# Kernel optimization log

Hardware: AMD Instinct MI355X
Metric: run time of the kernel (lower is better)

Reference implementation:

```python
import jax, jax.numpy as jnp
import numpy as np

B, H, T, D = 2, 16, 2048, 64


def setup_inputs() -> dict:
    key = jax.random.key(0)
    kq, kk, kv, km = jax.random.split(key, 4)
    q = jax.random.normal(kq, (B, H, T, D), dtype=jnp.float32)
    k = jax.random.normal(kk, (B, H, T, D), dtype=jnp.float32)
    v = jax.random.normal(kv, (B, H, T, D), dtype=jnp.float32)
    # boolean mask, True = masked out (broadcast over batch and heads)
    mask = jax.random.randint(km, (1, 1, T, T), 0, 2).astype(jnp.bool_)
    return {"q": q, "k": k, "v": v, "mask": mask}


def reference(q, k, v, mask):
    scale = q.shape[-1] ** (-0.5)
    # [B,H,T,T] score matrix (materialized, as in the original)
    scores = jnp.einsum("bhqd,bhkd->bhqk", q, k) * scale
    scores = jnp.where(mask, jnp.float32(-10000.0), scores)
    attn = jax.nn.softmax(scores, axis=-1)
    attn = jnp.where(mask, jnp.float32(0.0), attn)
    return jnp.einsum("bhqk,bhkd->bhqd", attn, v)
```

## Files before the change

kernel.cpp:

```cpp
#include <hip/hip_runtime.h>
#include <hip/hip_bf16.h>

typedef __bf16 bf16x8 __attribute__((ext_vector_type(8)));
typedef __bf16 bf16x4 __attribute__((ext_vector_type(4)));
typedef float  f32x4  __attribute__((ext_vector_type(4)));

#define T_SEQ 2048
#define D_HEAD 64
#define BH_N 32
#define NT_TILES (T_SEQ / 64)
#define QT_N 32
#define IMG_BYTES 16384
#define SCALE_LOG2 0.18033688011112042f

#define WS_IMG ((size_t)0)
#define WS_MB  ((size_t)16u << 20)

static __device__ __forceinline__ f32x4 mfma32(bf16x8 a, bf16x8 b, f32x4 c) {
    return __builtin_amdgcn_mfma_f32_16x16x32_bf16(a, b, c, 0, 0, 0);
}

static __device__ __forceinline__ float fast_exp2(float x) {
#if __has_builtin(__builtin_amdgcn_exp2f)
    return __builtin_amdgcn_exp2f(x);
#else
    return exp2f(x);
#endif
}

static __device__ __forceinline__ void gload16(const void* g, void* l, int lane) {
#if __has_builtin(__builtin_amdgcn_global_load_lds)
    (void)lane;
    __builtin_amdgcn_global_load_lds(
        (const __attribute__((address_space(1))) void*)g,
        (__attribute__((address_space(3))) void*)l, 16, 0, 0);
#else
    *((f32x4*)l + lane) = *(const f32x4*)g;
#endif
}


__global__ __launch_bounds__(256) void prep_kv(const float* __restrict__ k,
                                               const float* __restrict__ v,
                                               char* __restrict__ img) {
    __shared__ __bf16 t[64][72];
    const int bh = blockIdx.y, tt = blockIdx.x, tid = threadIdx.x;
    char* ob = img + ((size_t)bh * NT_TILES + tt) * IMG_BYTES;
    {
        const int kr = tid >> 2, qd = tid & 3, ke = kr & 7;
        const size_t base = ((size_t)bh * T_SEQ + tt * 64 + kr) * D_HEAD + qd * 16;
        const float4 a0 = *(const float4*)(k + base);
        const float4 a1 = *(const float4*)(k + base + 4);
        const float4 a2 = *(const float4*)(k + base + 8);
        const float4 a3 = *(const float4*)(k + base + 12);
        bf16x8 w0, w1;
        w0[0]=(__bf16)a0.x; w0[1]=(__bf16)a0.y; w0[2]=(__bf16)a0.z; w0[3]=(__bf16)a0.w;
        w0[4]=(__bf16)a1.x; w0[5]=(__bf16)a1.y; w0[6]=(__bf16)a1.z; w0[7]=(__bf16)a1.w;
        w1[0]=(__bf16)a2.x; w1[1]=(__bf16)a2.y; w1[2]=(__bf16)a2.z; w1[3]=(__bf16)a2.w;
        w1[4]=(__bf16)a3.x; w1[5]=(__bf16)a3.y; w1[6]=(__bf16)a3.z; w1[7]=(__bf16)a3.w;
        *(bf16x8*)(ob + kr * 128 + (((2 * qd + 0) ^ ke) << 4)) = w0;
        *(bf16x8*)(ob + kr * 128 + (((2 * qd + 1) ^ ke) << 4)) = w1;
    }
    {
        const int tr = tid >> 4, c4 = (tid & 15) * 4;
        const float* src = v + ((size_t)bh * T_SEQ + tt * 64) * D_HEAD;
#pragma unroll
        for (int p = 0; p < 4; ++p) {
            const int row = p * 16 + tr;
            const float4 f = *(const float4*)(src + row * D_HEAD + c4);
            t[c4+0][row] = (__bf16)f.x; t[c4+1][row] = (__bf16)f.y;
            t[c4+2][row] = (__bf16)f.z; t[c4+3][row] = (__bf16)f.w;
        }
        __syncthreads();
        const int d = tid >> 2;
        char* vb = ob + 8192 + d * 128;
#pragma unroll
        for (int mi = 0; mi < 2; ++mi) {
            const int m  = (tid & 3) * 2 + mi;
            const int u  = m ^ (d & 7);
            const int k0 = (u & 1) * 32 + (u >> 1) * 4;
            const bf16x4 lo = *(const bf16x4*)&t[d][k0];
            const bf16x4 hi = *(const bf16x4*)&t[d][k0 + 16];
            *(bf16x8*)(vb + m * 16) = __builtin_shufflevector(lo, hi, 0,1,2,3,4,5,6,7);
        }
    }
}

__global__ void mpack(const int* __restrict__ m, unsigned long long* __restrict__ mb) {
    const int i = blockIdx.x * 256 + threadIdx.x;
    const unsigned long long b = __ballot(m[i] != 0);
    if ((threadIdx.x & 63) == 0) mb[i >> 6] = b;
}


__global__ __launch_bounds__(512, 8) void attn12(
    const float* __restrict__ q, const char* __restrict__ img,
    const unsigned long long* __restrict__ mb, float* __restrict__ out)
{
    const int l   = blockIdx.x;
    const int bh  = ((l & 7) << 2) | ((l >> 3) & 3);
    const int qt  = l >> 5;

    const int tid = threadIdx.x, wave = tid >> 6, lane = tid & 63;
    const int g = lane >> 4, ln = lane & 15;
    const int qp = wave & 3, kh = wave >> 2;

    __shared__ __align__(16) char smem[33280];
    float* Ep = (float*)smem;
    float* Os = (float*)(smem + 32768);

    const int qw = qt * 64 + qp * 16;

    bf16x8 qf[2];
    {
        const float* qpt = q + ((size_t)bh * T_SEQ + qw + ln) * D_HEAD + g * 8;
#pragma unroll
        for (int kc = 0; kc < 2; ++kc) {
            const float4 f0 = *(const float4*)(qpt + kc * 32);
            const float4 f1 = *(const float4*)(qpt + kc * 32 + 4);
            qf[kc][0]=(__bf16)(f0.x*SCALE_LOG2); qf[kc][1]=(__bf16)(f0.y*SCALE_LOG2);
            qf[kc][2]=(__bf16)(f0.z*SCALE_LOG2); qf[kc][3]=(__bf16)(f0.w*SCALE_LOG2);
            qf[kc][4]=(__bf16)(f1.x*SCALE_LOG2); qf[kc][5]=(__bf16)(f1.y*SCALE_LOG2);
            qf[kc][6]=(__bf16)(f1.z*SCALE_LOG2); qf[kc][7]=(__bf16)(f1.w*SCALE_LOG2);
        }
    }

    f32x4 o[4];
#pragma unroll
    for (int mt = 0; mt < 4; ++mt) o[mt] = (f32x4){0.f, 0.f, 0.f, 0.f};
    f32x4 osum = (f32x4){0.f, 0.f, 0.f, 0.f};
    const bf16x8 ones8 = { (__bf16)1.0f, (__bf16)1.0f, (__bf16)1.0f, (__bf16)1.0f,
                           (__bf16)1.0f, (__bf16)1.0f, (__bf16)1.0f, (__bf16)1.0f };

    const char* ibase = img + (size_t)bh * (NT_TILES * (size_t)IMG_BYTES);
    const unsigned long long* mrow = mb + (size_t)(qw + ln) * 32;

    int koffs[2][2];
#pragma unroll
    for (int ntl = 0; ntl < 2; ++ntl) {
        const int row = (2 * kh + ntl) * 16 + ln;
        const int rb = row * 128 + ((g ^ (ln & 7)) << 4);
        koffs[ntl][0] = rb; koffs[ntl][1] = rb ^ 64;
    }
    int voffs[4];
#pragma unroll
    for (int mt = 0; mt < 4; ++mt)
        voffs[mt] = (mt * 16 + ln) * 128 + ((((g << 1) | kh) ^ (ln & 7)) << 4);

    char* buf0 = smem;
    char* buf1 = smem + 16384;

    auto stage = [&](int tile, char* dstbase) {
        const char* src = ibase + (size_t)tile * IMG_BYTES + wave * 2048 + lane * 16;
        char* dst = dstbase + wave * 2048;
        gload16(src, dst, lane);
        gload16(src + 1024, dst + 1024, lane);
    };

    auto compute_tile = [&](const char* KB, const char* VB, unsigned long long w0) {
        const unsigned nbs = (~(unsigned)(w0 >> (kh << 5))) >> (g * 4);

        bf16x8 pa8;
#pragma unroll
        for (int ntl = 0; ntl < 2; ++ntl) {
            const bf16x8 a0 = *(const bf16x8*)(KB + koffs[ntl][0]);
            const bf16x8 a1 = *(const bf16x8*)(KB + koffs[ntl][1]);
            f32x4 c = (f32x4){0.f, 0.f, 0.f, 0.f};
            __builtin_amdgcn_s_setprio(1);
            c = mfma32(a0, qf[0], c);
            c = mfma32(a1, qf[1], c);
            __builtin_amdgcn_s_setprio(0);
#pragma unroll
            for (int r = 0; r < 4; ++r) {
                const float e = fast_exp2(c[r]);
                const int keep = (int)(nbs << (31 - (ntl * 16 + r))) >> 31;
                const float p = __builtin_bit_cast(float,
                    __builtin_bit_cast(unsigned, e) & (unsigned)keep);
                pa8[ntl * 4 + r] = (__bf16)p;
            }
        }

        __builtin_amdgcn_s_setprio(1);
        osum = mfma32(pa8, ones8, osum);
#pragma unroll
        for (int mt = 0; mt < 4; ++mt) {
            const bf16x8 vv = *(const bf16x8*)(VB + voffs[mt]);
            o[mt] = mfma32(pa8, vv, o[mt]);
        }
        __builtin_amdgcn_s_setprio(0);
    };

    stage(0, buf0);
    unsigned long long mwA = mrow[0];
    __syncthreads();

#pragma unroll 1
    for (int i = 0; i < NT_TILES / 2; ++i) {
        const int t = 2 * i;
        stage(t + 1, buf1);
        const unsigned long long mwB = mrow[t + 1];
        compute_tile(buf0, buf0 + 8192, mwA);
        __syncthreads();
        if (i < NT_TILES / 2 - 1) {
            stage(t + 2, buf0);
            mwA = mrow[t + 2];
        }
        compute_tile(buf1, buf1 + 8192, mwB);
        __syncthreads();
    }

#pragma unroll
    for (int mt = 0; mt < 4; ++mt)
#pragma unroll
        for (int r = 0; r < 4; ++r)
            Ep[(size_t)kh * 4096 + (qp * 16 + g * 4 + r) * 64 + mt * 16 + ln] = o[mt][r];
    if (ln == 0) {
#pragma unroll
        for (int r = 0; r < 4; ++r)
            Os[kh * 64 + qp * 16 + g * 4 + r] = osum[r];
    }
    __syncthreads();
#pragma unroll
    for (int p2 = 0; p2 < 2; ++p2) {
        const int idx = p2 * 512 + tid;
        const int row = idx >> 4, c4 = (idx & 15) * 4;
        const float sl = Os[row] + Os[64 + row];
        const float inv = (sl > 0.f) ? (1.f / sl) : 0.f;
        const float4 a  = *(const float4*)(Ep + row * 64 + c4);
        const float4 b4 = *(const float4*)(Ep + 4096 + row * 64 + c4);
        const float4 st = { (a.x + b4.x) * inv, (a.y + b4.y) * inv,
                            (a.z + b4.z) * inv, (a.w + b4.w) * inv };
        *(float4*)(out + ((size_t)bh * T_SEQ + qt * 64 + row) * D_HEAD + c4) = st;
    }
}

extern "C" void kernel_launch(void* const* d_in, const int* in_sizes, int n_in,
                              void* d_out, int out_size, void* d_ws, size_t ws_size,
                              hipStream_t stream) {
    const float* q    = (const float*)d_in[0];
    const float* k    = (const float*)d_in[1];
    const float* v    = (const float*)d_in[2];
    const int*   mask = (const int*)d_in[3];
    float*       out  = (float*)d_out;

    char* img = (char*)d_ws + WS_IMG;
    unsigned long long* mbw = (unsigned long long*)((char*)d_ws + WS_MB);

    prep_kv<<<dim3(NT_TILES, BH_N), 256, 0, stream>>>(k, v, img);
    mpack<<<(T_SEQ * T_SEQ) / 256, 256, 0, stream>>>(mask, mbw);
    attn12<<<dim3(QT_N * BH_N), 512, 0, stream>>>(q, img, mbw, out);
}
```

Baseline: 166.2 us.

## Transpose packed mask to per-half-tile inverted words and hoist LDS fragment loads

The mask bitmap is now stored pre-inverted as 32-bit words in a transposed layout indexed by (tile half, query row). Each attention wave therefore loads only its own 32-bit word with coalesced lanes, instead of a 64-bit word strided by row. K and V fragment LDS reads are hoisted ahead of the MFMAs, and the keep mask uses a signed bitfield extract. The mask-pack kernel now does scattered 32-bit stores, and holding the hoisted fragments raises register pressure.

```diff
diff --git a/kernel.cpp b/kernel.cpp
--- a/kernel.cpp
+++ b/kernel.cpp
@@ -25,6 +25,14 @@
     return __builtin_amdgcn_exp2f(x);
 #else
     return exp2f(x);
+#endif
+}
+
+static __device__ __forceinline__ int sext_bit(unsigned w, int idx) {
+#if __has_builtin(__builtin_amdgcn_sbfe)
+    return __builtin_amdgcn_sbfe((int)w, idx, 1);
+#else
+    return (int)(w << (31 - idx)) >> 31;
 #endif
 }
 
@@ -86,16 +94,22 @@
     }
 }
 
-__global__ void mpack(const int* __restrict__ m, unsigned long long* __restrict__ mb) {
+__global__ void mpack(const int* __restrict__ m, unsigned* __restrict__ nbt) {
     const int i = blockIdx.x * 256 + threadIdx.x;
     const unsigned long long b = __ballot(m[i] != 0);
-    if ((threadIdx.x & 63) == 0) mb[i >> 6] = b;
-}
-
-
-__global__ __launch_bounds__(512, 8) void attn12(
+    if ((threadIdx.x & 63) == 0) {
+        const int wi  = i >> 6;
+        const int row = wi >> 5;
+        const int t   = wi & 31;
+        nbt[(size_t)(t * 2 + 0) * 2048 + row] = ~(unsigned)b;
+        nbt[(size_t)(t * 2 + 1) * 2048 + row] = ~(unsigned)(b >> 32);
+    }
+}
+
+
+__global__ __launch_bounds__(512, 8) void attn17(
     const float* __restrict__ q, const char* __restrict__ img,
-    const unsigned long long* __restrict__ mb, float* __restrict__ out)
+    const unsigned* __restrict__ nbt, float* __restrict__ out)
 {
     const int l   = blockIdx.x;
     const int bh  = ((l & 7) << 2) | ((l >> 3) & 3);
@@ -104,6 +118,7 @@
     const int tid = threadIdx.x, wave = tid >> 6, lane = tid & 63;
     const int g = lane >> 4, ln = lane & 15;
     const int qp = wave & 3, kh = wave >> 2;
+    const int g4 = g * 4;
 
     __shared__ __align__(16) char smem[33280];
     float* Ep = (float*)smem;
@@ -131,9 +146,10 @@
     f32x4 osum = (f32x4){0.f, 0.f, 0.f, 0.f};
     const bf16x8 ones8 = { (__bf16)1.0f, (__bf16)1.0f, (__bf16)1.0f, (__bf16)1.0f,
                            (__bf16)1.0f, (__bf16)1.0f, (__bf16)1.0f, (__bf16)1.0f };
+    const f32x4 z4 = (f32x4){0.f, 0.f, 0.f, 0.f};
 
     const char* ibase = img + (size_t)bh * (NT_TILES * (size_t)IMG_BYTES);
-    const unsigned long long* mrow = mb + (size_t)(qw + ln) * 32;
+    const unsigned* nb_base = nbt + (size_t)kh * 2048 + qw;
 
     int koffs[2][2];
 #pragma unroll
@@ -157,55 +173,61 @@
         gload16(src + 1024, dst + 1024, lane);
     };
 
-    auto compute_tile = [&](const char* KB, const char* VB, unsigned long long w0) {
-        const unsigned nbs = (~(unsigned)(w0 >> (kh << 5))) >> (g * 4);
+    auto compute_tile = [&](const char* KB, unsigned nw) {
+        const char* VB = KB + 8192;
+        const unsigned nbs = nw >> g4;
+
+        bf16x8 ka[2][2];
+#pragma unroll
+        for (int ntl = 0; ntl < 2; ++ntl) {
+            ka[ntl][0] = *(const bf16x8*)(KB + koffs[ntl][0]);
+            ka[ntl][1] = *(const bf16x8*)(KB + koffs[ntl][1]);
+        }
 
         bf16x8 pa8;
 #pragma unroll
         for (int ntl = 0; ntl < 2; ++ntl) {
-            const bf16x8 a0 = *(const bf16x8*)(KB + koffs[ntl][0]);
-            const bf16x8 a1 = *(const bf16x8*)(KB + koffs[ntl][1]);
-            f32x4 c = (f32x4){0.f, 0.f, 0.f, 0.f};
             __builtin_amdgcn_s_setprio(1);
-            c = mfma32(a0, qf[0], c);
-            c = mfma32(a1, qf[1], c);
+            f32x4 c = mfma32(ka[ntl][0], qf[0], z4);
+            c = mfma32(ka[ntl][1], qf[1], c);
             __builtin_amdgcn_s_setprio(0);
 #pragma unroll
             for (int r = 0; r < 4; ++r) {
                 const float e = fast_exp2(c[r]);
-                const int keep = (int)(nbs << (31 - (ntl * 16 + r))) >> 31;
+                const int keep = sext_bit(nbs, ntl * 16 + r);
                 const float p = __builtin_bit_cast(float,
                     __builtin_bit_cast(unsigned, e) & (unsigned)keep);
                 pa8[ntl * 4 + r] = (__bf16)p;
             }
         }
 
+        bf16x8 vv[4];
+#pragma unroll
+        for (int mt = 0; mt < 4; ++mt) vv[mt] = *(const bf16x8*)(VB + voffs[mt]);
         __builtin_amdgcn_s_setprio(1);
         osum = mfma32(pa8, ones8, osum);
 #pragma unroll
-        for (int mt = 0; mt < 4; ++mt) {
-            const bf16x8 vv = *(const bf16x8*)(VB + voffs[mt]);
-            o[mt] = mfma32(pa8, vv, o[mt]);
-        }
+        for (int mt = 0; mt < 4; ++mt)
+            o[mt] = mfma32(pa8, vv[mt], o[mt]);
         __builtin_amdgcn_s_setprio(0);
     };
 
     stage(0, buf0);
-    unsigned long long mwA = mrow[0];
+    unsigned mwA = nb_base[ln];
     __syncthreads();
 
 #pragma unroll 1
     for (int i = 0; i < NT_TILES / 2; ++i) {
         const int t = 2 * i;
         stage(t + 1, buf1);
-        const unsigned long long mwB = mrow[t + 1];
-        compute_tile(buf0, buf0 + 8192, mwA);
+        const unsigned mwB = nb_base[(size_t)(t + 1) * 4096 + ln];
+        compute_tile(buf0, mwA);
         __syncthreads();
         if (i < NT_TILES / 2 - 1) {
             stage(t + 2, buf0);
-            mwA = mrow[t + 2];
-        }
-        compute_tile(buf1, buf1 + 8192, mwB);
+            mwA = nb_base[(size_t)(t + 2) * 4096 + ln];
+        }
+        compute_tile(buf1, mwB);
         __syncthreads();
     }
 
@@ -244,9 +266,9 @@
     float*       out  = (float*)d_out;
 
     char* img = (char*)d_ws + WS_IMG;
-    unsigned long long* mbw = (unsigned long long*)((char*)d_ws + WS_MB);
+    unsigned* nbt = (unsigned*)((char*)d_ws + WS_MB);
 
     prep_kv<<<dim3(NT_TILES, BH_N), 256, 0, stream>>>(k, v, img);
-    mpack<<<(T_SEQ * T_SEQ) / 256, 256, 0, stream>>>(mask, mbw);
-    attn12<<<dim3(QT_N * BH_N), 512, 0, stream>>>(q, img, mbw, out);
-}
+    mpack<<<(T_SEQ * T_SEQ) / 256, 256, 0, stream>>>(mask, nbt);
+    attn17<<<dim3(QT_N * BH_N), 512, 0, stream>>>(q, img, nbt, out);
+}
```

Result: slower. 169.9 us (+2.2%).
